# Optimization experiments

Hardware: AMD Instinct MI355X
Metric: run time of the kernel (lower is better)

## Reference

```python
import jax, jax.numpy as jnp
import numpy as np

TAU = 2.0          # LIF membrane time constant
VTH = 1.0          # spike threshold
ALPHA = 2.0        # ATan surrogate default alpha
EPS = 1e-5         # LayerNorm eps


@jax.custom_vjp
def atan_spike(x):
    # Heaviside forward, ATan surrogate gradient backward (spikingjelly surrogate.ATan)
    return (x >= 0.0).astype(x.dtype)

def _spike_fwd(x):
    return atan_spike(x), x

def _spike_bwd(x, g):
    sg = (ALPHA / 2.0) / (1.0 + (jnp.pi / 2.0 * ALPHA * x) ** 2)
    return (g * sg,)

atan_spike.defvjp(_spike_fwd, _spike_bwd)


def lif_scan(xs):
    # xs: [T, B, C]; multi-step LIF with decay_input=True, v_reset=0.0 (hard reset),
    # detach_reset=True (reset path is stop_gradient'ed).
    def step(v, x):
        h = v + (x - v) / TAU                      # charge
        s = atan_spike(h - VTH)                    # fire
        v_new = h * (1.0 - jax.lax.stop_gradient(s))  # hard reset to 0, detached
        return v_new, s
    _, spikes = jax.lax.scan(step, jnp.zeros_like(xs[0]), xs)
    return spikes


def setup_inputs() -> dict:
    key = jax.random.key(0)
    ks = jax.random.split(key, 5)
    B, T, D, H = 32, 2048, 128, 256
    x = jax.random.normal(ks[0], (B, T, D), dtype=jnp.float32)
    W1 = jax.random.normal(ks[1], (H, D), dtype=jnp.float32) * (1.0 / np.sqrt(D))
    b1 = jax.random.normal(ks[2], (H,), dtype=jnp.float32) * 0.02
    W2 = jax.random.normal(ks[3], (D, H), dtype=jnp.float32) * (1.0 / np.sqrt(H))
    b2 = jax.random.normal(ks[4], (D,), dtype=jnp.float32) * 0.02
    ln_w = jnp.ones((D,), dtype=jnp.float32)
    ln_b = jnp.zeros((D,), dtype=jnp.float32)
    return {"x": x, "W1": W1, "b1": b1, "W2": W2, "b2": b2, "ln_w": ln_w, "ln_b": ln_b}


def reference(x, W1, b1, W2, b2, ln_w, ln_b):
    # x: [B, T, D] -> time-major [T, B, D]
    h = jnp.swapaxes(x, 0, 1)
    h = h @ W1.T + b1            # [T, B, H]
    h = lif_scan(h)              # spikes in {0,1}
    h = h @ W2.T + b2            # [T, B, D]
    h = lif_scan(h)
    h = jnp.swapaxes(h, 0, 1)    # back to [B, T, D]
    y = x + h                    # residual
    mu = jnp.mean(y, axis=-1, keepdims=True)
    var = jnp.mean((y - mu) ** 2, axis=-1, keepdims=True)
    return (y - mu) * jax.lax.rsqrt(var + EPS) * ln_w + ln_b
```

## Files before the change

kernel.cpp:

```cpp
#include <hip/hip_runtime.h>


typedef _Float16 half8 __attribute__((ext_vector_type(8)));
typedef float f32x4 __attribute__((ext_vector_type(4)));

#define MFMA_F16(a, b, c) __builtin_amdgcn_mfma_f32_16x16x32_f16(a, b, c, 0, 0, 0)

__device__ __forceinline__ unsigned short h2u(_Float16 h) {
    union { _Float16 h; unsigned short u; } x; x.h = h; return x.u;
}

__device__ __forceinline__ void split8(float4 f0, float4 f1, half8& a, half8& b) {
    float fs[8] = {f0.x, f0.y, f0.z, f0.w, f1.x, f1.y, f1.z, f1.w};
    half8 ha, hb;
#pragma unroll
    for (int q = 0; q < 8; ++q) {
        ha[q] = (_Float16)fs[q];
        hb[q] = (_Float16)(fs[q] - (float)ha[q]);
    }
    a = ha; b = hb;
}

__global__ __launch_bounds__(512, 1) void mega_kernel(
    const float* __restrict__ X,
    const float* __restrict__ W1, const float* __restrict__ W2,
    const float* __restrict__ b1, const float* __restrict__ b2,
    const float* __restrict__ lnw, const float* __restrict__ lnb,
    float* __restrict__ out)
{
    __shared__ __align__(16) float hbuf[2][16 * 260];
    __shared__ __align__(16) unsigned short xabuf[2][2][16 * 136];

    const int tid = threadIdx.x;
    const int lane = tid & 63;
    const int w = tid >> 6;
    const bool isS = (tid < 256);
    const int sg = w;
    const int gg = w - 4;
    const int fr = lane & 15;
    const int fo8 = (lane >> 4) * 8;
    const int qr = (lane >> 4) * 4;
    const int b = blockIdx.y;
    const int t0 = blockIdx.x * 256;
    const int s0 = (blockIdx.x == 0) ? 8 : 0;

    const float* __restrict__ xbase = X + (size_t)b * 2048 * 128;
    float* __restrict__ obase = out + (size_t)b * 2048 * 128;

    half8 wf[32];
    float bias0[4];
    if (isS) {
#pragma unroll
        for (int j = 0; j < 2; ++j) {
            const size_t d = (size_t)(32 * sg + 16 * j + fr) * 256;
#pragma unroll
            for (int ks = 0; ks < 8; ++ks) {
                float4 f0 = *(const float4*)&W2[d + ks * 32 + fo8];
                float4 f1 = *(const float4*)&W2[d + ks * 32 + fo8 + 4];
                split8(f0, f1, wf[(j * 8 + ks) * 2], wf[(j * 8 + ks) * 2 + 1]);
            }
            bias0[j] = b2[32 * sg + 16 * j + fr];
        }
    } else {
#pragma unroll
        for (int j = 0; j < 4; ++j) {
            const size_t n = (size_t)(64 * gg + 16 * j + fr) * 128;
#pragma unroll
            for (int k0 = 0; k0 < 4; ++k0) {
                float4 f0 = *(const float4*)&W1[n + k0 * 32 + fo8];
                float4 f1 = *(const float4*)&W1[n + k0 * 32 + fo8 + 4];
                split8(f0, f1, wf[(j * 4 + k0) * 2], wf[(j * 4 + k0) * 2 + 1]);
            }
            bias0[j] = b1[64 * gg + 16 * j + fr];
        }
    }
    const float2 wv = *(const float2*)(lnw + lane * 2);
    const float2 bbv = *(const float2*)(lnb + lane * 2);

    float v1 = 0.0f, v2 = 0.0f;
    float4 pfx[2];
    const int tg = tid & 255;
    const int prow = tg >> 5;
    const int pc4 = (tg & 31) * 4;

    if (!isS) {
        const int tb0 = t0 - 128 + s0 * 16;
#pragma unroll
        for (int q = 0; q < 2; ++q) {
            float4 xv = *(const float4*)&xbase[(size_t)(tb0 + prow + q * 8) * 128 + pc4];
            half8 a, e; split8(xv, xv, a, e);
            _Float16 a0 = (_Float16)xv.x, e0 = (_Float16)(xv.x - (float)a0);
            _Float16 a1 = (_Float16)xv.y, e1 = (_Float16)(xv.y - (float)a1);
            _Float16 a2 = (_Float16)xv.z, e2 = (_Float16)(xv.z - (float)a2);
            _Float16 a3 = (_Float16)xv.w, e3 = (_Float16)(xv.w - (float)a3);
            ushort4 ua = {h2u(a0), h2u(a1), h2u(a2), h2u(a3)};
            ushort4 ue = {h2u(e0), h2u(e1), h2u(e2), h2u(e3)};
            *(ushort4*)&xabuf[s0 & 1][0][(prow + q * 8) * 136 + pc4] = ua;
            *(ushort4*)&xabuf[s0 & 1][1][(prow + q * 8) * 136 + pc4] = ue;
        }
#pragma unroll
        for (int q = 0; q < 2; ++q)
            pfx[q] = *(const float4*)&xbase[(size_t)(tb0 + 16 + prow + q * 8) * 128 + pc4];
    }
    __syncthreads();
    if (!isS) {
        const _Float16* xa0 = (const _Float16*)&xabuf[s0 & 1][0][0];
        const _Float16* xa1 = (const _Float16*)&xabuf[s0 & 1][1][0];
        f32x4 acc[4];
#pragma unroll
        for (int j = 0; j < 4; ++j) acc[j] = (f32x4){0.f, 0.f, 0.f, 0.f};
#pragma unroll
        for (int k0 = 0; k0 < 4; ++k0) {
            half8 a0 = *(const half8*)&xa0[fr * 136 + k0 * 32 + fo8];
            half8 a1 = *(const half8*)&xa1[fr * 136 + k0 * 32 + fo8];
#pragma unroll
            for (int j = 0; j < 4; ++j) {
                acc[j] = MFMA_F16(a0, wf[(j * 4 + k0) * 2], acc[j]);
                acc[j] = MFMA_F16(a0, wf[(j * 4 + k0) * 2 + 1], acc[j]);
                acc[j] = MFMA_F16(a1, wf[(j * 4 + k0) * 2], acc[j]);
            }
        }
#pragma unroll
        for (int j = 0; j < 4; ++j) {
            int col = 64 * gg + 16 * j + fr;
#pragma unroll
            for (int r = 0; r < 4; ++r)
                hbuf[s0 & 1][(qr + r) * 260 + col] = acc[j][r] + bias0[j];
        }
    }
    __syncthreads();

    for (int s = s0; s < 24; ++s) {
        const int tbase = t0 - 128 + s * 16;
        const bool mainsub = (s >= 8);

        if (isS) {
            unsigned short* spk = &xabuf[s & 1][0][0];
            float hh[16];
#pragma unroll
            for (int t = 0; t < 16; ++t) hh[t] = hbuf[s & 1][t * 260 + tid];
#pragma unroll
            for (int t = 0; t < 16; ++t) {
                float h = v1 + (hh[t] - v1) * 0.5f;
                bool sp = (h >= 1.0f);
                v1 = sp ? 0.0f : h;
                spk[t * 264 + tid] = sp ? (unsigned short)0x3C00 : (unsigned short)0;
            }
        } else if (s < 23) {
#pragma unroll
            for (int q = 0; q < 2; ++q) {
                float4 xv = pfx[q];
                _Float16 a0 = (_Float16)xv.x, e0 = (_Float16)(xv.x - (float)a0);
                _Float16 a1 = (_Float16)xv.y, e1 = (_Float16)(xv.y - (float)a1);
                _Float16 a2 = (_Float16)xv.z, e2 = (_Float16)(xv.z - (float)a2);
                _Float16 a3 = (_Float16)xv.w, e3 = (_Float16)(xv.w - (float)a3);
                ushort4 ua = {h2u(a0), h2u(a1), h2u(a2), h2u(a3)};
                ushort4 ue = {h2u(e0), h2u(e1), h2u(e2), h2u(e3)};
                *(ushort4*)&xabuf[(s + 1) & 1][0][(prow + q * 8) * 136 + pc4] = ua;
                *(ushort4*)&xabuf[(s + 1) & 1][1][(prow + q * 8) * 136 + pc4] = ue;
            }
        }
        __syncthreads();

        float2 pfln[2];
        if (mainsub) {
#pragma unroll
            for (int rr = 0; rr < 2; ++rr)
                pfln[rr] = *(const float2*)&xbase[(size_t)(tbase + 2 * w + rr) * 128 + lane * 2];
        }
        if (isS) {
            const _Float16* sp = (const _Float16*)&xabuf[s & 1][0][0];
            f32x4 acc[2];
            acc[0] = (f32x4){0.f, 0.f, 0.f, 0.f};
            acc[1] = (f32x4){0.f, 0.f, 0.f, 0.f};
#pragma unroll
            for (int ks = 0; ks < 8; ++ks) {
                half8 a = *(const half8*)&sp[fr * 264 + ks * 32 + fo8];
#pragma unroll
                for (int j = 0; j < 2; ++j) {
                    acc[j] = MFMA_F16(a, wf[(j * 8 + ks) * 2], acc[j]);
                    acc[j] = MFMA_F16(a, wf[(j * 8 + ks) * 2 + 1], acc[j]);
                }
            }
#pragma unroll
            for (int j = 0; j < 2; ++j) {
                int col = 32 * sg + 16 * j + fr;
#pragma unroll
                for (int r = 0; r < 4; ++r)
                    hbuf[s & 1][(qr + r) * 260 + col] = acc[j][r] + bias0[j];
            }
        } else if (s < 23) {
            const _Float16* xa0 = (const _Float16*)&xabuf[(s + 1) & 1][0][0];
            const _Float16* xa1 = (const _Float16*)&xabuf[(s + 1) & 1][1][0];
            f32x4 acc[4];
#pragma unroll
            for (int j = 0; j < 4; ++j) acc[j] = (f32x4){0.f, 0.f, 0.f, 0.f};
#pragma unroll
            for (int k0 = 0; k0 < 4; ++k0) {
                half8 a0 = *(const half8*)&xa0[fr * 136 + k0 * 32 + fo8];
                half8 a1 = *(const half8*)&xa1[fr * 136 + k0 * 32 + fo8];
#pragma unroll
                for (int j = 0; j < 4; ++j) {
                    acc[j] = MFMA_F16(a0, wf[(j * 4 + k0) * 2], acc[j]);
                    acc[j] = MFMA_F16(a0, wf[(j * 4 + k0) * 2 + 1], acc[j]);
                    acc[j] = MFMA_F16(a1, wf[(j * 4 + k0) * 2], acc[j]);
                }
            }
#pragma unroll
            for (int j = 0; j < 4; ++j) {
                int col = 64 * gg + 16 * j + fr;
#pragma unroll
                for (int r = 0; r < 4; ++r)
                    hbuf[(s + 1) & 1][(qr + r) * 260 + col] = acc[j][r] + bias0[j];
            }
            if (s < 22) {
#pragma unroll
                for (int q = 0; q < 2; ++q)
                    pfx[q] = *(const float4*)&xbase[(size_t)(tbase + 32 + prow + q * 8) * 128 + pc4];
            }
        }
        __syncthreads();

        if (tid < 128) {
            float hh[16];
#pragma unroll
            for (int t = 0; t < 16; ++t) hh[t] = hbuf[s & 1][t * 260 + tid];
#pragma unroll
            for (int t = 0; t < 16; ++t) {
                float h = v2 + (hh[t] - v2) * 0.5f;
                bool sp = (h >= 1.0f);
                v2 = sp ? 0.0f : h;
                if (mainsub) hbuf[s & 1][t * 260 + tid] = sp ? 1.0f : 0.0f;
            }
        }

        if (mainsub) {
            __syncthreads();
#pragma unroll
            for (int rr = 0; rr < 2; ++rr) {
                int row = 2 * w + rr;
                float2 s2v = *(const float2*)&hbuf[s & 1][row * 260 + lane * 2];
                float y0 = pfln[rr].x + s2v.x;
                float y1 = pfln[rr].y + s2v.y;
                float sum = y0 + y1;
                float ss = y0 * y0 + y1 * y1;
#pragma unroll
                for (int off = 32; off > 0; off >>= 1) {
                    sum += __shfl_xor(sum, off, 64);
                    ss  += __shfl_xor(ss, off, 64);
                }
                float mu = sum * (1.0f / 128.0f);
                float var = ss * (1.0f / 128.0f) - mu * mu;
                float inv = rsqrtf(var + 1e-5f);
                float2 o;
                o.x = (y0 - mu) * inv * wv.x + bbv.x;
                o.y = (y1 - mu) * inv * wv.y + bbv.y;
                *(float2*)&obase[(size_t)(tbase + row) * 128 + lane * 2] = o;
            }
        }
    }
}

extern "C" void kernel_launch(void* const* d_in, const int* in_sizes, int n_in,
                              void* d_out, int out_size, void* d_ws, size_t ws_size,
                              hipStream_t stream)
{
    const float* x   = (const float*)d_in[0];
    const float* W1  = (const float*)d_in[1];
    const float* b1  = (const float*)d_in[2];
    const float* W2  = (const float*)d_in[3];
    const float* b2  = (const float*)d_in[4];
    const float* lnw = (const float*)d_in[5];
    const float* lnb = (const float*)d_in[6];
    float* out = (float*)d_out;

    dim3 gM(8, 32);
    mega_kernel<<<gM, 512, 0, stream>>>(x, W1, W2, b1, b2, lnw, lnb, out);
}
```

Measured before the change: 150.4 us.

## Software-pipeline LIF2 and LayerNorm one stage behind with dedicated warp roles

Restructures the per-step schedule so that the second LIF scan runs on waves 4-5 and the LayerNorm epilogue for the previous 16-row chunk runs one iteration late. This overlaps them with the GEMMs and drops one or two barriers per step, leaving two __syncthreads per iteration. The x conversion and prefetch are moved onto only the last two waves with a single x buffer. Separate h1/h2/s2/spike buffers replace the double-buffered shared arrays. The cost is one extra loop iteration, and serial scan work lands on waves that also do GEMM.

```diff
diff --git a/kernel.cpp b/kernel.cpp
--- a/kernel.cpp
+++ b/kernel.cpp
@@ -28,8 +28,11 @@
     const float* __restrict__ lnw, const float* __restrict__ lnb,
     float* __restrict__ out)
 {
-    __shared__ __align__(16) float hbuf[2][16 * 260];
-    __shared__ __align__(16) unsigned short xabuf[2][2][16 * 136];
+    __shared__ __align__(16) float h1buf[16 * 260];
+    __shared__ __align__(16) float h2buf[16 * 132];
+    __shared__ __align__(16) float s2buf[16 * 132];
+    __shared__ __align__(16) unsigned short spkbuf[16 * 264];
+    __shared__ __align__(16) unsigned short xb[2][16 * 136];
 
     const int tid = threadIdx.x;
     const int lane = tid & 63;
@@ -78,34 +81,32 @@
     const float2 bbv = *(const float2*)(lnb + lane * 2);
 
     float v1 = 0.0f, v2 = 0.0f;
-    float4 pfx[2];
-    const int tg = tid & 255;
-    const int prow = tg >> 5;
-    const int pc4 = (tg & 31) * 4;
-
-    if (!isS) {
-        const int tb0 = t0 - 128 + s0 * 16;
-#pragma unroll
-        for (int q = 0; q < 2; ++q) {
-            float4 xv = *(const float4*)&xbase[(size_t)(tb0 + prow + q * 8) * 128 + pc4];
-            half8 a, e; split8(xv, xv, a, e);
+    const int d2 = (tid - 256) & 127;
+    const int tgs = (tid - 384) & 127;
+    const int srow = tgs >> 5;
+    const int sc4 = (tgs & 31) * 4;
+    float4 pfx[4];
+    float2 pflnC[2], pflnN[2];
+
+    if (tid >= 384) {
+        const int tb = t0 - 128 + s0 * 16;
+#pragma unroll
+        for (int q = 0; q < 4; ++q) {
+            float4 xv = *(const float4*)&xbase[(size_t)(tb + srow + 4 * q) * 128 + sc4];
             _Float16 a0 = (_Float16)xv.x, e0 = (_Float16)(xv.x - (float)a0);
             _Float16 a1 = (_Float16)xv.y, e1 = (_Float16)(xv.y - (float)a1);
             _Float16 a2 = (_Float16)xv.z, e2 = (_Float16)(xv.z - (float)a2);
             _Float16 a3 = (_Float16)xv.w, e3 = (_Float16)(xv.w - (float)a3);
             ushort4 ua = {h2u(a0), h2u(a1), h2u(a2), h2u(a3)};
             ushort4 ue = {h2u(e0), h2u(e1), h2u(e2), h2u(e3)};
-            *(ushort4*)&xabuf[s0 & 1][0][(prow + q * 8) * 136 + pc4] = ua;
-            *(ushort4*)&xabuf[s0 & 1][1][(prow + q * 8) * 136 + pc4] = ue;
-        }
-#pragma unroll
-        for (int q = 0; q < 2; ++q)
-            pfx[q] = *(const float4*)&xbase[(size_t)(tb0 + 16 + prow + q * 8) * 128 + pc4];
+            *(ushort4*)&xb[0][(srow + 4 * q) * 136 + sc4] = ua;
+            *(ushort4*)&xb[1][(srow + 4 * q) * 136 + sc4] = ue;
+        }
     }
     __syncthreads();
     if (!isS) {
-        const _Float16* xa0 = (const _Float16*)&xabuf[s0 & 1][0][0];
-        const _Float16* xa1 = (const _Float16*)&xabuf[s0 & 1][1][0];
+        const _Float16* xa0 = (const _Float16*)&xb[0][0];
+        const _Float16* xa1 = (const _Float16*)&xb[1][0];
         f32x4 acc[4];
 #pragma unroll
         for (int j = 0; j < 4; ++j) acc[j] = (f32x4){0.f, 0.f, 0.f, 0.f};
@@ -125,123 +126,134 @@
             int col = 64 * gg + 16 * j + fr;
 #pragma unroll
             for (int r = 0; r < 4; ++r)
-                hbuf[s0 & 1][(qr + r) * 260 + col] = acc[j][r] + bias0[j];
+                h1buf[(qr + r) * 260 + col] = acc[j][r] + bias0[j];
+        }
+        if (tid >= 384) {
+            const int tb = t0 - 128 + s0 * 16 + 16;
+#pragma unroll
+            for (int q = 0; q < 4; ++q)
+                pfx[q] = *(const float4*)&xbase[(size_t)(tb + srow + 4 * q) * 128 + sc4];
         }
     }
     __syncthreads();
 
-    for (int s = s0; s < 24; ++s) {
+    for (int s = s0; s <= 24; ++s) {
         const int tbase = t0 - 128 + s * 16;
-        const bool mainsub = (s >= 8);
 
         if (isS) {
-            unsigned short* spk = &xabuf[s & 1][0][0];
-            float hh[16];
-#pragma unroll
-            for (int t = 0; t < 16; ++t) hh[t] = hbuf[s & 1][t * 260 + tid];
-#pragma unroll
-            for (int t = 0; t < 16; ++t) {
-                float h = v1 + (hh[t] - v1) * 0.5f;
-                bool sp = (h >= 1.0f);
-                v1 = sp ? 0.0f : h;
-                spk[t * 264 + tid] = sp ? (unsigned short)0x3C00 : (unsigned short)0;
-            }
-        } else if (s < 23) {
-#pragma unroll
-            for (int q = 0; q < 2; ++q) {
-                float4 xv = pfx[q];
-                _Float16 a0 = (_Float16)xv.x, e0 = (_Float16)(xv.x - (float)a0);
-                _Float16 a1 = (_Float16)xv.y, e1 = (_Float16)(xv.y - (float)a1);
-                _Float16 a2 = (_Float16)xv.z, e2 = (_Float16)(xv.z - (float)a2);
-                _Float16 a3 = (_Float16)xv.w, e3 = (_Float16)(xv.w - (float)a3);
-                ushort4 ua = {h2u(a0), h2u(a1), h2u(a2), h2u(a3)};
-                ushort4 ue = {h2u(e0), h2u(e1), h2u(e2), h2u(e3)};
-                *(ushort4*)&xabuf[(s + 1) & 1][0][(prow + q * 8) * 136 + pc4] = ua;
-                *(ushort4*)&xabuf[(s + 1) & 1][1][(prow + q * 8) * 136 + pc4] = ue;
+            if (s <= 23) {
+                float hh[16];
+#pragma unroll
+                for (int t = 0; t < 16; ++t) hh[t] = h1buf[t * 260 + tid];
+#pragma unroll
+                for (int t = 0; t < 16; ++t) {
+                    float h = v1 + (hh[t] - v1) * 0.5f;
+                    bool sp = (h >= 1.0f);
+                    v1 = sp ? 0.0f : h;
+                    spkbuf[t * 264 + tid] = sp ? (unsigned short)0x3C00 : (unsigned short)0;
+                }
+            }
+        } else if (tid < 384) {
+            if (s > s0) {
+                float hh[16];
+#pragma unroll
+                for (int t = 0; t < 16; ++t) hh[t] = h2buf[t * 132 + d2];
+#pragma unroll
+                for (int t = 0; t < 16; ++t) {
+                    float h = v2 + (hh[t] - v2) * 0.5f;
+                    bool sp = (h >= 1.0f);
+                    v2 = sp ? 0.0f : h;
+                    s2buf[t * 132 + d2] = sp ? 1.0f : 0.0f;
+                }
+            }
+        } else {
+            if (s <= 22) {
+#pragma unroll
+                for (int q = 0; q < 4; ++q) {
+                    float4 xv = pfx[q];
+                    _Float16 a0 = (_Float16)xv.x, e0 = (_Float16)(xv.x - (float)a0);
+                    _Float16 a1 = (_Float16)xv.y, e1 = (_Float16)(xv.y - (float)a1);
+                    _Float16 a2 = (_Float16)xv.z, e2 = (_Float16)(xv.z - (float)a2);
+                    _Float16 a3 = (_Float16)xv.w, e3 = (_Float16)(xv.w - (float)a3);
+                    ushort4 ua = {h2u(a0), h2u(a1), h2u(a2), h2u(a3)};
+                    ushort4 ue = {h2u(e0), h2u(e1), h2u(e2), h2u(e3)};
+                    *(ushort4*)&xb[0][(srow + 4 * q) * 136 + sc4] = ua;
+                    *(ushort4*)&xb[1][(srow + 4 * q) * 136 + sc4] = ue;
+                }
             }
         }
         __syncthreads();
 
-        float2 pfln[2];
-        if (mainsub) {
+        if (isS) {
+            if (s <= 23) {
+                const _Float16* sp = (const _Float16*)&spkbuf[0];
+                f32x4 acc[2];
+                acc[0] = (f32x4){0.f, 0.f, 0.f, 0.f};
+                acc[1] = (f32x4){0.f, 0.f, 0.f, 0.f};
+#pragma unroll
+                for (int ks = 0; ks < 8; ++ks) {
+                    half8 a = *(const half8*)&sp[fr * 264 + ks * 32 + fo8];
+#pragma unroll
+                    for (int j = 0; j < 2; ++j) {
+                        acc[j] = MFMA_F16(a, wf[(j * 8 + ks) * 2], acc[j]);
+                        acc[j] = MFMA_F16(a, wf[(j * 8 + ks) * 2 + 1], acc[j]);
+                    }
+                }
+#pragma unroll
+                for (int j = 0; j < 2; ++j) {
+                    int col = 32 * sg + 16 * j + fr;
+#pragma unroll
+                    for (int r = 0; r < 4; ++r)
+                        h2buf[(qr + r) * 132 + col] = acc[j][r] + bias0[j];
+                }
+            }
+        } else {
+            if (s <= 22) {
+                const _Float16* xa0 = (const _Float16*)&xb[0][0];
+                const _Float16* xa1 = (const _Float16*)&xb[1][0];
+                f32x4 acc[4];
+#pragma unroll
+                for (int j = 0; j < 4; ++j) acc[j] = (f32x4){0.f, 0.f, 0.f, 0.f};
+#pragma unroll
+                for (int k0 = 0; k0 < 4; ++k0) {
+                    half8 a0 = *(const half8*)&xa0[fr * 136 + k0 * 32 + fo8];
+                    half8 a1 = *(const half8*)&xa1[fr * 136 + k0 * 32 + fo8];
+#pragma unroll
+                    for (int j = 0; j < 4; ++j) {
+                        acc[j] = MFMA_F16(a0, wf[(j * 4 + k0) * 2], acc[j]);
+                        acc[j] = MFMA_F16(a0, wf[(j * 4 + k0) * 2 + 1], acc[j]);
+                        acc[j] = MFMA_F16(a1, wf[(j * 4 + k0) * 2], acc[j]);
+                    }
+                }
+#pragma unroll
+                for (int j = 0; j < 4; ++j) {
+                    int col = 64 * gg + 16 * j + fr;
+#pragma unroll
+                    for (int r = 0; r < 4; ++r)
+                        h1buf[(qr + r) * 260 + col] = acc[j][r] + bias0[j];
+                }
+            }
+            if (tid >= 384 && s <= 21) {
+#pragma unroll
+                for (int q = 0; q < 4; ++q)
+                    pfx[q] = *(const float4*)&xbase[(size_t)(tbase + 32 + srow + 4 * q) * 128 + sc4];
+            }
+        }
+
+        if (s >= 8 && s <= 23) {
 #pragma unroll
             for (int rr = 0; rr < 2; ++rr)
-                pfln[rr] = *(const float2*)&xbase[(size_t)(tbase + 2 * w + rr) * 128 + lane * 2];
-        }
-        if (isS) {
-            const _Float16* sp = (const _Float16*)&xabuf[s & 1][0][0];
-            f32x4 acc[2];
-            acc[0] = (f32x4){0.f, 0.f, 0.f, 0.f};
-            acc[1] = (f32x4){0.f, 0.f, 0.f, 0.f};
-#pragma unroll
-            for (int ks = 0; ks < 8; ++ks) {
-                half8 a = *(const half8*)&sp[fr * 264 + ks * 32 + fo8];
-#pragma unroll
-                for (int j = 0; j < 2; ++j) {
-                    acc[j] = MFMA_F16(a, wf[(j * 8 + ks) * 2], acc[j]);
-                    acc[j] = MFMA_F16(a, wf[(j * 8 + ks) * 2 + 1], acc[j]);
-                }
-            }
-#pragma unroll
-            for (int j = 0; j < 2; ++j) {
-                int col = 32 * sg + 16 * j + fr;
-#pragma unroll
-                for (int r = 0; r < 4; ++r)
-                    hbuf[s & 1][(qr + r) * 260 + col] = acc[j][r] + bias0[j];
-            }
-        } else if (s < 23) {
-            const _Float16* xa0 = (const _Float16*)&xabuf[(s + 1) & 1][0][0];
-            const _Float16* xa1 = (const _Float16*)&xabuf[(s + 1) & 1][1][0];
-            f32x4 acc[4];
-#pragma unroll
-            for (int j = 0; j < 4; ++j) acc[j] = (f32x4){0.f, 0.f, 0.f, 0.f};
-#pragma unroll
-            for (int k0 = 0; k0 < 4; ++k0) {
-                half8 a0 = *(const half8*)&xa0[fr * 136 + k0 * 32 + fo8];
-                half8 a1 = *(const half8*)&xa1[fr * 136 + k0 * 32 + fo8];
-#pragma unroll
-                for (int j = 0; j < 4; ++j) {
-                    acc[j] = MFMA_F16(a0, wf[(j * 4 + k0) * 2], acc[j]);
-                    acc[j] = MFMA_F16(a0, wf[(j * 4 + k0) * 2 + 1], acc[j]);
-                    acc[j] = MFMA_F16(a1, wf[(j * 4 + k0) * 2], acc[j]);
-                }
-            }
-#pragma unroll
-            for (int j = 0; j < 4; ++j) {
-                int col = 64 * gg + 16 * j + fr;
-#pragma unroll
-                for (int r = 0; r < 4; ++r)
-                    hbuf[(s + 1) & 1][(qr + r) * 260 + col] = acc[j][r] + bias0[j];
-            }
-            if (s < 22) {
-#pragma unroll
-                for (int q = 0; q < 2; ++q)
-                    pfx[q] = *(const float4*)&xbase[(size_t)(tbase + 32 + prow + q * 8) * 128 + pc4];
-            }
-        }
-        __syncthreads();
-
-        if (tid < 128) {
-            float hh[16];
-#pragma unroll
-            for (int t = 0; t < 16; ++t) hh[t] = hbuf[s & 1][t * 260 + tid];
-#pragma unroll
-            for (int t = 0; t < 16; ++t) {
-                float h = v2 + (hh[t] - v2) * 0.5f;
-                bool sp = (h >= 1.0f);
-                v2 = sp ? 0.0f : h;
-                if (mainsub) hbuf[s & 1][t * 260 + tid] = sp ? 1.0f : 0.0f;
-            }
-        }
-
-        if (mainsub) {
-            __syncthreads();
+                pflnN[rr] = *(const float2*)&xbase[(size_t)(tbase + 2 * w + rr) * 128 + lane * 2];
+        }
+
+        if (s >= 9) {
+            const int tbm = tbase - 16;
 #pragma unroll
             for (int rr = 0; rr < 2; ++rr) {
                 int row = 2 * w + rr;
-                float2 s2v = *(const float2*)&hbuf[s & 1][row * 260 + lane * 2];
-                float y0 = pfln[rr].x + s2v.x;
-                float y1 = pfln[rr].y + s2v.y;
+                float2 s2v = *(const float2*)&s2buf[row * 132 + lane * 2];
+                float y0 = pflnC[rr].x + s2v.x;
+                float y1 = pflnC[rr].y + s2v.y;
                 float sum = y0 + y1;
                 float ss = y0 * y0 + y1 * y1;
 #pragma unroll
@@ -255,9 +267,12 @@
                 float2 o;
                 o.x = (y0 - mu) * inv * wv.x + bbv.x;
                 o.y = (y1 - mu) * inv * wv.y + bbv.y;
-                *(float2*)&obase[(size_t)(tbase + row) * 128 + lane * 2] = o;
-            }
-        }
+                *(float2*)&obase[(size_t)(tbm + row) * 128 + lane * 2] = o;
+            }
+        }
+        pflnC[0] = pflnN[0];
+        pflnC[1] = pflnN[1];
+        __syncthreads();
     }
 }
 
```

Result: faster. 144.2 us (-4.1%).
